# Kernel optimization log

Hardware: AMD Instinct MI355X
Metric: run time of the kernel (lower is better)

## Reference

```python
import jax, jax.numpy as jnp
import numpy as np

B, C, T, F = 64, 128, 2048, 5
ALPHA, BETA = 0.5, 0.5
N = C * F  # 640 nodes


def _spatial_adjacency():
    # |i-j| <= 3 neighbors within each frequency band block (block diagonal)
    idx = np.arange(C)
    d = np.abs(idx[:, None] - idx[None, :])
    blk = ((d <= 3) & (d > 0)).astype(np.float32)
    return jnp.asarray(np.kron(np.eye(F, dtype=np.float32), blk))


A_SPATIAL = _spatial_adjacency()  # (N, N)


def setup_inputs() -> dict:
    key = jax.random.key(0)
    ks = jax.random.split(key, 5)
    names = ['delta', 'theta', 'alpha', 'beta', 'gamma']
    return {n: jax.random.normal(k, (B, C, T), dtype=jnp.float32) for n, k in zip(names, ks)}


def _strg(delta, theta, alpha, beta, gamma):
    bands = jnp.stack([delta, theta, alpha, beta, gamma], axis=1)  # (B, F, C, T)
    Bn, Fn, Cn, Tn = bands.shape

    # bandpower = unbiased variance over time (torch.var default ddof=1)
    bp = jnp.var(bands, axis=3, ddof=1)  # (B, F, C)
    bandpowers = jnp.transpose(bp, (0, 2, 1))  # (B, C, F)
    # node ordering: node f*C + ch -> bandpowers[b, ch, f] == bp[b, f, ch]
    node_features = bp.reshape(Bn, Fn * Cn, 1)

    # Pearson-style functional connectivity per batch & band (vectorized)
    mean = jnp.mean(bands, axis=3, keepdims=True)
    std = jnp.std(bands, axis=3, ddof=1, keepdims=True)  # torch.std unbiased
    xn = (bands - mean) / (std + 1e-8)
    corr = jnp.einsum('bfct,bfdt->bfcd', xn, xn) / (Tn - 1)  # (B, F, C, C)
    corr = jnp.abs(corr)
    eye = jnp.eye(Cn, dtype=corr.dtype)
    corr = corr * (1.0 - eye) + eye  # zero diag, then set diag = 1
    corr = 0.5 * (corr + jnp.swapaxes(corr, 2, 3))

    # block-diagonal assembly into full functional adjacency
    A_func = jnp.zeros((Bn, N, N), dtype=corr.dtype)
    for f in range(Fn):
        s = f * Cn
        A_func = A_func.at[:, s:s + Cn, s:s + Cn].set(corr[:, f])

    A = ALPHA * A_SPATIAL[None] + BETA * A_func  # (B, N, N)

    # symmetric degree normalization D^-1/2 A D^-1/2
    D = jnp.sum(A, axis=2)
    d_inv_sqrt = (D + 1e-8) ** -0.5
    d_inv_sqrt = jnp.where(jnp.isinf(d_inv_sqrt), 0.0, d_inv_sqrt)
    A_norm = d_inv_sqrt[:, :, None] * A * d_inv_sqrt[:, None, :]

    return A_norm, node_features, bandpowers


def reference(delta, theta, alpha, beta, gamma):
    return _strg(delta, theta, alpha, beta, gamma)
```

## Files before the change

### kernel.cpp

```cpp
#include <hip/hip_runtime.h>
#include <hip/hip_bf16.h>

#define Bn 64
#define Cn 128
#define Tn 2048
#define Fn 5
#define Nn 640
#define TCHUNK 128
#define NCHUNK (Tn / TCHUNK)

typedef __attribute__((ext_vector_type(8))) short bf16x8;
typedef __attribute__((ext_vector_type(4))) float f32x4;

__device__ __forceinline__ short f2bf(float f) {
    union { float f; unsigned u; } v; v.f = f;
    unsigned r = (v.u + 0x7fffu + ((v.u >> 16) & 1u)) >> 16;
    return (short)r;
}

__device__ __forceinline__ int swz_off(int row, int bytecol) {
    return (row * 256 + bytecol) ^ ((row & 7) << 4);
}

__global__ __launch_bounds__(512)
void strg_kernel(const float* __restrict__ d0, const float* __restrict__ d1,
                 const float* __restrict__ d2, const float* __restrict__ d3,
                 const float* __restrict__ d4, float* __restrict__ out)
{
    __shared__ short  Xs[Cn * TCHUNK];
    __shared__ float  S_lds[Cn];
    __shared__ float  diag[Cn];
    __shared__ float  mrow[Cn];
    __shared__ float  ivrow[Cn];
    __shared__ float  D_lds[Cn];
    __shared__ float  dinv[Cn];

    const int tid = threadIdx.x;
    const int bfid = blockIdx.x;
    const int b = bfid / Fn;
    const int f = bfid - b * Fn;

    const float* src = (f == 0) ? d0 : (f == 1) ? d1 : (f == 2) ? d2 : (f == 3) ? d3 : d4;
    src += (size_t)b * Cn * Tn;

    if (tid < Cn) { S_lds[tid] = 0.0f; D_lds[tid] = 0.0f; }

    const int srow = tid >> 4;
    const int sseg = tid & 15;

    const int lane = tid & 63;
    const int w  = tid >> 6;
    const int wr = w >> 1;
    const int wc = w & 1;
    const int r0 = wr * 32;
    const int c0 = wc * 64;
    const int lg = lane >> 4;
    const int ll = lane & 15;

    f32x4 acc[2][4] = {};
    float psum[4] = {0.f, 0.f, 0.f, 0.f};

    for (int ch = 0; ch < NCHUNK; ++ch) {
        const float* cb = src + ch * TCHUNK;
        #pragma unroll
        for (int i = 0; i < 4; ++i) {
            const int row = i * 32 + srow;
            const float* rp = cb + (size_t)row * Tn + sseg * 8;
            float4 v0 = *(const float4*)rp;
            float4 v1 = *(const float4*)(rp + 4);
            psum[i] += v0.x + v0.y + v0.z + v0.w + v1.x + v1.y + v1.z + v1.w;
            bf16x8 h;
            h[0]=f2bf(v0.x); h[1]=f2bf(v0.y); h[2]=f2bf(v0.z); h[3]=f2bf(v0.w);
            h[4]=f2bf(v1.x); h[5]=f2bf(v1.y); h[6]=f2bf(v1.z); h[7]=f2bf(v1.w);
            *(bf16x8*)((char*)Xs + swz_off(row, sseg * 16)) = h;
        }
        __syncthreads();

        #pragma unroll
        for (int ks = 0; ks < 4; ++ks) {
            bf16x8 afr[2], bfr[4];
            #pragma unroll
            for (int m = 0; m < 2; ++m) {
                const int row = r0 + m * 16 + ll;
                afr[m] = *(const bf16x8*)((const char*)Xs + swz_off(row, ks * 64 + lg * 16));
            }
            #pragma unroll
            for (int n = 0; n < 4; ++n) {
                const int col = c0 + n * 16 + ll;
                bfr[n] = *(const bf16x8*)((const char*)Xs + swz_off(col, ks * 64 + lg * 16));
            }
            #pragma unroll
            for (int m = 0; m < 2; ++m)
                #pragma unroll
                for (int n = 0; n < 4; ++n)
                    acc[m][n] = __builtin_amdgcn_mfma_f32_16x16x32_bf16(afr[m], bfr[n], acc[m][n], 0, 0, 0);
        }
        __syncthreads();
    }

    #pragma unroll
    for (int i = 0; i < 4; ++i)
        atomicAdd(&S_lds[i * 32 + srow], psum[i]);

    #pragma unroll
    for (int m = 0; m < 2; ++m)
      #pragma unroll
      for (int n = 0; n < 4; ++n)
        #pragma unroll
        for (int e = 0; e < 4; ++e) {
            const int row = r0 + m * 16 + lg * 4 + e;
            const int col = c0 + n * 16 + ll;
            if (row == col) diag[row] = acc[m][n][e];
        }
    __syncthreads();

    if (tid < Cn) {
        const float S  = S_lds[tid];
        const float mu = S * (1.0f / Tn);
        float var = (diag[tid] - (float)Tn * mu * mu) * (1.0f / (Tn - 1));
        var = var < 0.f ? 0.f : var;
        const float sd = sqrtf(var);
        mrow[tid]  = mu;
        ivrow[tid] = 1.0f / (sd + 1e-8f);
        const size_t ofs = (size_t)Bn * Nn * Nn;
        out[ofs + (size_t)b * Nn + f * Cn + tid] = var;
        out[ofs + (size_t)Bn * Nn + ((size_t)b * Cn + tid) * Fn + f] = var;
    }
    __syncthreads();

    float mi[2][4], ii[2][4], mj[4], ij[4];
    #pragma unroll
    for (int m = 0; m < 2; ++m)
      #pragma unroll
      for (int e = 0; e < 4; ++e) {
          const int row = r0 + m * 16 + lg * 4 + e;
          mi[m][e] = mrow[row];
          ii[m][e] = ivrow[row];
      }
    #pragma unroll
    for (int n = 0; n < 4; ++n) {
        const int col = c0 + n * 16 + ll;
        mj[n] = mrow[col];
        ij[n] = ivrow[col];
    }

    auto ablk = [&](int m, int n, int e) -> float {
        const int row = r0 + m * 16 + lg * 4 + e;
        const int col = c0 + n * 16 + ll;
        float c = fabsf((acc[m][n][e] - (float)Tn * mi[m][e] * mj[n])
                        * ii[m][e] * ij[n] * (1.0f / (Tn - 1)));
        c = (row == col) ? 1.0f : c;
        const int d = row > col ? row - col : col - row;
        const float spa = (d >= 1 && d <= 3) ? 1.0f : 0.0f;
        return 0.5f * (spa + c);
    };

    #pragma unroll
    for (int m = 0; m < 2; ++m)
      #pragma unroll
      for (int e = 0; e < 4; ++e) {
          float s = 0.f;
          #pragma unroll
          for (int n = 0; n < 4; ++n) s += ablk(m, n, e);
          s += __shfl_xor(s, 1);
          s += __shfl_xor(s, 2);
          s += __shfl_xor(s, 4);
          s += __shfl_xor(s, 8);
          if (ll == 0) atomicAdd(&D_lds[r0 + m * 16 + lg * 4 + e], s);
      }
    __syncthreads();

    if (tid < Cn) dinv[tid] = rsqrtf(D_lds[tid] + 1e-8f);
    __syncthreads();

    float di[2][4], dj[4];
    #pragma unroll
    for (int m = 0; m < 2; ++m)
      #pragma unroll
      for (int e = 0; e < 4; ++e)
          di[m][e] = dinv[r0 + m * 16 + lg * 4 + e];
    #pragma unroll
    for (int n = 0; n < 4; ++n)
        dj[n] = dinv[c0 + n * 16 + ll];

    float* Ab = out + (size_t)b * Nn * Nn;
    const int fc = f * Cn;
    #pragma unroll
    for (int m = 0; m < 2; ++m)
      #pragma unroll
      for (int e = 0; e < 4; ++e) {
          const int row = r0 + m * 16 + lg * 4 + e;
          const size_t rowoff = (size_t)(fc + row) * Nn + fc;
          #pragma unroll
          for (int n = 0; n < 4; ++n) {
              const int col = c0 + n * 16 + ll;
              Ab[rowoff + col] = di[m][e] * ablk(m, n, e) * dj[n];
          }
      }
}

extern "C" void kernel_launch(void* const* d_in, const int* in_sizes, int n_in,
                              void* d_out, int out_size, void* d_ws, size_t ws_size,
                              hipStream_t stream) {
    const float* d0 = (const float*)d_in[0];
    const float* d1 = (const float*)d_in[1];
    const float* d2 = (const float*)d_in[2];
    const float* d3 = (const float*)d_in[3];
    const float* d4 = (const float*)d_in[4];
    float* out = (float*)d_out;

    hipMemsetAsync(d_out, 0, (size_t)out_size * sizeof(float), stream);

    strg_kernel<<<dim3(Bn * Fn), dim3(512), 0, stream>>>(d0, d1, d2, d3, d4, out);
}
```

Before: 113.5 us.

## Split Gram computation over time chunks and finalize in a separate kernel

```diff
diff --git a/kernel.cpp b/kernel.cpp
--- a/kernel.cpp
+++ b/kernel.cpp
@@ -7,7 +7,6 @@
 #define Fn 5
 #define Nn 640
 #define TCHUNK 128
-#define NCHUNK (Tn / TCHUNK)
 
 typedef __attribute__((ext_vector_type(8))) short bf16x8;
 typedef __attribute__((ext_vector_type(4))) float f32x4;
@@ -22,10 +21,213 @@
     return (row * 256 + bytecol) ^ ((row & 7) << 4);
 }
 
+__device__ __forceinline__ const float* pick_band(const float* d0, const float* d1,
+                                                  const float* d2, const float* d3,
+                                                  const float* d4, int f) {
+    return (f == 0) ? d0 : (f == 1) ? d1 : (f == 2) ? d2 : (f == 3) ? d3 : d4;
+}
+
+__global__ __launch_bounds__(512, 4)
+void gram_kernel(const float* __restrict__ d0, const float* __restrict__ d1,
+                 const float* __restrict__ d2, const float* __restrict__ d3,
+                 const float* __restrict__ d4,
+                 float* __restrict__ wsG, float* __restrict__ wsS, int Q)
+{
+    __shared__ short Xs[Cn * TCHUNK];
+    __shared__ float S_lds[Cn];
+
+    const int tid = threadIdx.x;
+    const int blk = blockIdx.x;
+    const int bf = blk / Q;
+    const int q  = blk - bf * Q;
+    const int b = bf / Fn;
+    const int f = bf - b * Fn;
+    const int NC = 16 / Q;
+
+    const float* src = pick_band(d0, d1, d2, d3, d4, f)
+                     + (size_t)b * Cn * Tn + (size_t)q * (Tn / Q);
+
+    if (tid < Cn) S_lds[tid] = 0.0f;
+
+    const int srow = tid >> 4;
+    const int sseg = tid & 15;
+
+    const int lane = tid & 63;
+    const int w  = tid >> 6;
+    const int wr = w >> 1;
+    const int wc = w & 1;
+    const int r0 = wr * 32;
+    const int c0 = wc * 64;
+    const int lg = lane >> 4;
+    const int ll = lane & 15;
+
+    f32x4 acc[2][4] = {};
+    float psum[4] = {0.f, 0.f, 0.f, 0.f};
+
+    float4 pf[8];
+    auto issue = [&](int ch) {
+        const float* cb = src + ch * TCHUNK;
+        #pragma unroll
+        for (int i = 0; i < 4; ++i) {
+            const float* rp = cb + (size_t)(i * 32 + srow) * Tn + sseg * 8;
+            pf[2 * i]     = *(const float4*)rp;
+            pf[2 * i + 1] = *(const float4*)(rp + 4);
+        }
+    };
+
+    issue(0);
+
+    for (int ch = 0; ch < NC; ++ch) {
+        #pragma unroll
+        for (int i = 0; i < 4; ++i) {
+            const int row = i * 32 + srow;
+            float4 v0 = pf[2 * i], v1 = pf[2 * i + 1];
+            psum[i] += v0.x + v0.y + v0.z + v0.w + v1.x + v1.y + v1.z + v1.w;
+            bf16x8 h;
+            h[0]=f2bf(v0.x); h[1]=f2bf(v0.y); h[2]=f2bf(v0.z); h[3]=f2bf(v0.w);
+            h[4]=f2bf(v1.x); h[5]=f2bf(v1.y); h[6]=f2bf(v1.z); h[7]=f2bf(v1.w);
+            *(bf16x8*)((char*)Xs + swz_off(row, sseg * 16)) = h;
+        }
+        if (ch + 1 < NC) issue(ch + 1);
+        __syncthreads();
+
+        #pragma unroll
+        for (int ks = 0; ks < 4; ++ks) {
+            bf16x8 afr[2], bfr[4];
+            #pragma unroll
+            for (int m = 0; m < 2; ++m) {
+                const int row = r0 + m * 16 + ll;
+                afr[m] = *(const bf16x8*)((const char*)Xs + swz_off(row, ks * 64 + lg * 16));
+            }
+            #pragma unroll
+            for (int n = 0; n < 4; ++n) {
+                const int col = c0 + n * 16 + ll;
+                bfr[n] = *(const bf16x8*)((const char*)Xs + swz_off(col, ks * 64 + lg * 16));
+            }
+            #pragma unroll
+            for (int m = 0; m < 2; ++m)
+                #pragma unroll
+                for (int n = 0; n < 4; ++n)
+                    acc[m][n] = __builtin_amdgcn_mfma_f32_16x16x32_bf16(afr[m], bfr[n], acc[m][n], 0, 0, 0);
+        }
+        __syncthreads();
+    }
+
+    #pragma unroll
+    for (int i = 0; i < 4; ++i)
+        atomicAdd(&S_lds[i * 32 + srow], psum[i]);
+    __syncthreads();
+    if (tid < Cn) wsS[(size_t)blk * Cn + tid] = S_lds[tid];
+
+    float* G = wsG + (size_t)blk * (Cn * Cn);
+    #pragma unroll
+    for (int m = 0; m < 2; ++m)
+      #pragma unroll
+      for (int e = 0; e < 4; ++e) {
+          const int row = r0 + m * 16 + lg * 4 + e;
+          #pragma unroll
+          for (int n = 0; n < 4; ++n) {
+              const int col = c0 + n * 16 + ll;
+              G[row * Cn + col] = acc[m][n][e];
+          }
+      }
+}
+
+__global__ __launch_bounds__(256)
+void finalize_kernel(const float* __restrict__ wsG, const float* __restrict__ wsS,
+                     float* __restrict__ out, int Q)
+{
+    __shared__ float G[Cn * Cn];
+    __shared__ float mrow[Cn], ivrow[Cn], dinv_s[Cn], Dsum[Cn];
+
+    const int tid = threadIdx.x;
+    const int bf = blockIdx.x;
+    const int b = bf / Fn;
+    const int f = bf - b * Fn;
+
+    const float* P0 = wsG + (size_t)bf * Q * (Cn * Cn);
+    for (int e = 0; e < 16; ++e) {
+        const int idx = e * 1024 + tid * 4;
+        float4 s = *(const float4*)(P0 + idx);
+        for (int qq = 1; qq < Q; ++qq) {
+            float4 t = *(const float4*)(P0 + (size_t)qq * (Cn * Cn) + idx);
+            s.x += t.x; s.y += t.y; s.z += t.z; s.w += t.w;
+        }
+        *(float4*)&G[idx] = s;
+    }
+
+    float S = 0.f;
+    if (tid < Cn) {
+        const float* Sp = wsS + (size_t)bf * Q * Cn;
+        for (int qq = 0; qq < Q; ++qq) S += Sp[qq * Cn + tid];
+        Dsum[tid] = 0.f;
+    }
+    __syncthreads();
+
+    if (tid < Cn) {
+        const float mu = S * (1.0f / Tn);
+        float var = (G[tid * (Cn + 1)] - (float)Tn * mu * mu) * (1.0f / (Tn - 1));
+        var = var < 0.f ? 0.f : var;
+        const float sd = sqrtf(var);
+        mrow[tid]  = mu;
+        ivrow[tid] = 1.0f / (sd + 1e-8f);
+        const size_t ofs = (size_t)Bn * Nn * Nn;
+        out[ofs + (size_t)b * Nn + f * Cn + tid] = var;
+        out[ofs + (size_t)Bn * Nn + ((size_t)b * Cn + tid) * Fn + f] = var;
+    }
+    __syncthreads();
+
+    const float inv = 1.0f / (Tn - 1);
+    for (int e = 0; e < 64; ++e) {
+        const int idx = e * 256 + tid;
+        const int row = idx >> 7;
+        const int col = idx & 127;
+        const float qv = G[idx];
+        float c = fabsf((qv - (float)Tn * mrow[row] * mrow[col]) * ivrow[row] * ivrow[col] * inv);
+        c = (row == col) ? 1.0f : c;
+        const int d = row > col ? row - col : col - row;
+        const float spa = (d >= 1 && d <= 3) ? 1.0f : 0.0f;
+        const float a = 0.5f * (spa + c);
+        G[idx] = a;
+        float s = a;
+        s += __shfl_xor(s, 1);
+        s += __shfl_xor(s, 2);
+        s += __shfl_xor(s, 4);
+        s += __shfl_xor(s, 8);
+        s += __shfl_xor(s, 16);
+        s += __shfl_xor(s, 32);
+        if ((tid & 63) == 0) atomicAdd(&Dsum[row], s);
+    }
+    __syncthreads();
+
+    if (tid < Cn) dinv_s[tid] = rsqrtf(Dsum[tid] + 1e-8f);
+    __syncthreads();
+
+    float* Ob = out + (size_t)b * Nn * Nn;
+    const int fc = f * Cn;
+    for (int e = 0; e < 80; ++e) {
+        const int idx4 = e * 1024 + tid * 4;
+        const int row = idx4 / Nn;
+        const int col = idx4 - row * Nn;
+        const int cl = col - fc;
+        float4 v;
+        if (cl >= 0 && cl < Cn) {
+            const float dr = dinv_s[row];
+            v.x = dr * G[row * Cn + cl]     * dinv_s[cl];
+            v.y = dr * G[row * Cn + cl + 1] * dinv_s[cl + 1];
+            v.z = dr * G[row * Cn + cl + 2] * dinv_s[cl + 2];
+            v.w = dr * G[row * Cn + cl + 3] * dinv_s[cl + 3];
+        } else {
+            v.x = 0.f; v.y = 0.f; v.z = 0.f; v.w = 0.f;
+        }
+        *(float4*)(Ob + (size_t)(fc + row) * Nn + col) = v;
+    }
+}
+
 __global__ __launch_bounds__(512)
-void strg_kernel(const float* __restrict__ d0, const float* __restrict__ d1,
-                 const float* __restrict__ d2, const float* __restrict__ d3,
-                 const float* __restrict__ d4, float* __restrict__ out)
+void strg_fallback(const float* __restrict__ d0, const float* __restrict__ d1,
+                   const float* __restrict__ d2, const float* __restrict__ d3,
+                   const float* __restrict__ d4, float* __restrict__ out)
 {
     __shared__ short  Xs[Cn * TCHUNK];
     __shared__ float  S_lds[Cn];
@@ -40,14 +242,12 @@
     const int b = bfid / Fn;
     const int f = bfid - b * Fn;
 
-    const float* src = (f == 0) ? d0 : (f == 1) ? d1 : (f == 2) ? d2 : (f == 3) ? d3 : d4;
-    src += (size_t)b * Cn * Tn;
+    const float* src = pick_band(d0, d1, d2, d3, d4, f) + (size_t)b * Cn * Tn;
 
     if (tid < Cn) { S_lds[tid] = 0.0f; D_lds[tid] = 0.0f; }
 
     const int srow = tid >> 4;
     const int sseg = tid & 15;
-
     const int lane = tid & 63;
     const int w  = tid >> 6;
     const int wr = w >> 1;
@@ -60,7 +260,7 @@
     f32x4 acc[2][4] = {};
     float psum[4] = {0.f, 0.f, 0.f, 0.f};
 
-    for (int ch = 0; ch < NCHUNK; ++ch) {
+    for (int ch = 0; ch < 16; ++ch) {
         const float* cb = src + ch * TCHUNK;
         #pragma unroll
         for (int i = 0; i < 4; ++i) {
@@ -75,20 +275,15 @@
             *(bf16x8*)((char*)Xs + swz_off(row, sseg * 16)) = h;
         }
         __syncthreads();
-
         #pragma unroll
         for (int ks = 0; ks < 4; ++ks) {
             bf16x8 afr[2], bfr[4];
             #pragma unroll
-            for (int m = 0; m < 2; ++m) {
-                const int row = r0 + m * 16 + ll;
-                afr[m] = *(const bf16x8*)((const char*)Xs + swz_off(row, ks * 64 + lg * 16));
-            }
-            #pragma unroll
-            for (int n = 0; n < 4; ++n) {
-                const int col = c0 + n * 16 + ll;
-                bfr[n] = *(const bf16x8*)((const char*)Xs + swz_off(col, ks * 64 + lg * 16));
-            }
+            for (int m = 0; m < 2; ++m)
+                afr[m] = *(const bf16x8*)((const char*)Xs + swz_off(r0 + m * 16 + ll, ks * 64 + lg * 16));
+            #pragma unroll
+            for (int n = 0; n < 4; ++n)
+                bfr[n] = *(const bf16x8*)((const char*)Xs + swz_off(c0 + n * 16 + ll, ks * 64 + lg * 16));
             #pragma unroll
             for (int m = 0; m < 2; ++m)
                 #pragma unroll
@@ -209,7 +404,19 @@
     const float* d4 = (const float*)d_in[4];
     float* out = (float*)d_out;
 
-    hipMemsetAsync(d_out, 0, (size_t)out_size * sizeof(float), stream);
-
-    strg_kernel<<<dim3(Bn * Fn), dim3(512), 0, stream>>>(d0, d1, d2, d3, d4, out);
-}
+    int Q = 0;
+    for (int cand = 4; cand >= 1; cand >>= 1) {
+        size_t need = (size_t)320 * cand * (Cn * Cn + Cn) * sizeof(float);
+        if (need <= ws_size) { Q = cand; break; }
+    }
+
+    if (Q > 0) {
+        float* wsG = (float*)d_ws;
+        float* wsS = wsG + (size_t)320 * Q * (Cn * Cn);
+        gram_kernel<<<dim3(320 * Q), dim3(512), 0, stream>>>(d0, d1, d2, d3, d4, wsG, wsS, Q);
+        finalize_kernel<<<dim3(320), dim3(256), 0, stream>>>(wsG, wsS, out, Q);
+    } else {
+        hipMemsetAsync(d_out, 0, (size_t)out_size * sizeof(float), stream);
+        strg_fallback<<<dim3(320), dim3(512), 0, stream>>>(d0, d1, d2, d3, d4, out);
+    }
+}
```

Result: slower. 170.8 us (+50.6%).

## Double-buffer input staging and fuse zero-fill into coalesced output writes

Applied to the files above, without the earlier changes.

```diff
diff --git a/kernel.cpp b/kernel.cpp
--- a/kernel.cpp
+++ b/kernel.cpp
@@ -7,7 +7,8 @@
 #define Fn 5
 #define Nn 640
 #define TCHUNK 128
-#define NCHUNK (Tn / TCHUNK)
+#define NCHUNK 16
+#define BUFBYTES (Cn * TCHUNK * 2)
 
 typedef __attribute__((ext_vector_type(8))) short bf16x8;
 typedef __attribute__((ext_vector_type(4))) float f32x4;
@@ -22,28 +23,27 @@
     return (row * 256 + bytecol) ^ ((row & 7) << 4);
 }
 
-__global__ __launch_bounds__(512)
-void strg_kernel(const float* __restrict__ d0, const float* __restrict__ d1,
-                 const float* __restrict__ d2, const float* __restrict__ d3,
-                 const float* __restrict__ d4, float* __restrict__ out)
+__device__ __forceinline__ const float* pick_band(const float* d0, const float* d1,
+                                                  const float* d2, const float* d3,
+                                                  const float* d4, int f) {
+    return (f == 0) ? d0 : (f == 1) ? d1 : (f == 2) ? d2 : (f == 3) ? d3 : d4;
+}
+
+__global__ __launch_bounds__(512, 4)
+void strg_mono(const float* __restrict__ d0, const float* __restrict__ d1,
+               const float* __restrict__ d2, const float* __restrict__ d3,
+               const float* __restrict__ d4, float* __restrict__ out)
 {
-    __shared__ short  Xs[Cn * TCHUNK];
-    __shared__ float  S_lds[Cn];
-    __shared__ float  diag[Cn];
-    __shared__ float  mrow[Cn];
-    __shared__ float  ivrow[Cn];
-    __shared__ float  D_lds[Cn];
-    __shared__ float  dinv[Cn];
+    __shared__ __align__(16) char smem[2 * BUFBYTES];
+    __shared__ float S_lds[Cn], diag[Cn], mrow[Cn], ivrow[Cn], Dsum[Cn], dinv_s[Cn];
 
     const int tid = threadIdx.x;
     const int bfid = blockIdx.x;
     const int b = bfid / Fn;
     const int f = bfid - b * Fn;
-
-    const float* src = (f == 0) ? d0 : (f == 1) ? d1 : (f == 2) ? d2 : (f == 3) ? d3 : d4;
-    src += (size_t)b * Cn * Tn;
-
-    if (tid < Cn) { S_lds[tid] = 0.0f; D_lds[tid] = 0.0f; }
+    const float* src = pick_band(d0, d1, d2, d3, d4, f) + (size_t)b * Cn * Tn;
+
+    if (tid < Cn) { S_lds[tid] = 0.0f; Dsum[tid] = 0.0f; }
 
     const int srow = tid >> 4;
     const int sseg = tid & 15;
@@ -59,43 +59,68 @@
 
     f32x4 acc[2][4] = {};
     float psum[4] = {0.f, 0.f, 0.f, 0.f};
-
-    for (int ch = 0; ch < NCHUNK; ++ch) {
-        const float* cb = src + ch * TCHUNK;
+    float4 pf[8];
+
+    const float* tb0 = src + (size_t)srow * Tn + sseg * 8;
+
+    auto issue = [&](int ch) {
+        const float* cb = tb0 + ch * TCHUNK;
+        #pragma unroll
+        for (int i = 0; i < 4; ++i) {
+            const float* rp = cb + (size_t)(i * 32) * Tn;
+            pf[2 * i]     = *(const float4*)rp;
+            pf[2 * i + 1] = *(const float4*)(rp + 4);
+        }
+    };
+    auto convert_write = [&](int buf) {
+        char* base = smem + buf * BUFBYTES;
         #pragma unroll
         for (int i = 0; i < 4; ++i) {
             const int row = i * 32 + srow;
-            const float* rp = cb + (size_t)row * Tn + sseg * 8;
-            float4 v0 = *(const float4*)rp;
-            float4 v1 = *(const float4*)(rp + 4);
+            float4 v0 = pf[2 * i], v1 = pf[2 * i + 1];
             psum[i] += v0.x + v0.y + v0.z + v0.w + v1.x + v1.y + v1.z + v1.w;
             bf16x8 h;
             h[0]=f2bf(v0.x); h[1]=f2bf(v0.y); h[2]=f2bf(v0.z); h[3]=f2bf(v0.w);
             h[4]=f2bf(v1.x); h[5]=f2bf(v1.y); h[6]=f2bf(v1.z); h[7]=f2bf(v1.w);
-            *(bf16x8*)((char*)Xs + swz_off(row, sseg * 16)) = h;
-        }
-        __syncthreads();
-
+            *(bf16x8*)(base + swz_off(row, sseg * 16)) = h;
+        }
+    };
+    auto mfma_phase = [&](int buf) {
+        const char* base = smem + buf * BUFBYTES;
         #pragma unroll
         for (int ks = 0; ks < 4; ++ks) {
             bf16x8 afr[2], bfr[4];
             #pragma unroll
-            for (int m = 0; m < 2; ++m) {
-                const int row = r0 + m * 16 + ll;
-                afr[m] = *(const bf16x8*)((const char*)Xs + swz_off(row, ks * 64 + lg * 16));
-            }
+            for (int m = 0; m < 2; ++m)
+                afr[m] = *(const bf16x8*)(base + swz_off(r0 + m * 16 + ll, ks * 64 + lg * 16));
             #pragma unroll
-            for (int n = 0; n < 4; ++n) {
-                const int col = c0 + n * 16 + ll;
-                bfr[n] = *(const bf16x8*)((const char*)Xs + swz_off(col, ks * 64 + lg * 16));
-            }
+            for (int n = 0; n < 4; ++n)
+                bfr[n] = *(const bf16x8*)(base + swz_off(c0 + n * 16 + ll, ks * 64 + lg * 16));
             #pragma unroll
             for (int m = 0; m < 2; ++m)
                 #pragma unroll
                 for (int n = 0; n < 4; ++n)
                     acc[m][n] = __builtin_amdgcn_mfma_f32_16x16x32_bf16(afr[m], bfr[n], acc[m][n], 0, 0, 0);
         }
-        __syncthreads();
+    };
+
+    issue(0);
+    convert_write(0);
+    issue(1);
+    asm volatile("s_waitcnt lgkmcnt(0)" ::: "memory");
+    __builtin_amdgcn_s_barrier();
+    __builtin_amdgcn_sched_barrier(0);
+
+    for (int ch = 0; ch < NCHUNK; ++ch) {
+        const int cur = ch & 1;
+        mfma_phase(cur);
+        if (ch + 1 < NCHUNK) {
+            convert_write(cur ^ 1);
+            if (ch + 2 < NCHUNK) issue(ch + 2);
+        }
+        asm volatile("s_waitcnt lgkmcnt(0)" ::: "memory");
+        __builtin_amdgcn_s_barrier();
+        __builtin_amdgcn_sched_barrier(0);
     }
 
     #pragma unroll
@@ -128,75 +153,71 @@
     }
     __syncthreads();
 
-    float mi[2][4], ii[2][4], mj[4], ij[4];
-    #pragma unroll
-    for (int m = 0; m < 2; ++m)
-      #pragma unroll
-      for (int e = 0; e < 4; ++e) {
-          const int row = r0 + m * 16 + lg * 4 + e;
-          mi[m][e] = mrow[row];
-          ii[m][e] = ivrow[row];
-      }
-    #pragma unroll
-    for (int n = 0; n < 4; ++n) {
-        const int col = c0 + n * 16 + ll;
-        mj[n] = mrow[col];
-        ij[n] = ivrow[col];
-    }
-
-    auto ablk = [&](int m, int n, int e) -> float {
-        const int row = r0 + m * 16 + lg * 4 + e;
-        const int col = c0 + n * 16 + ll;
-        float c = fabsf((acc[m][n][e] - (float)Tn * mi[m][e] * mj[n])
-                        * ii[m][e] * ij[n] * (1.0f / (Tn - 1)));
-        c = (row == col) ? 1.0f : c;
-        const int d = row > col ? row - col : col - row;
-        const float spa = (d >= 1 && d <= 3) ? 1.0f : 0.0f;
-        return 0.5f * (spa + c);
-    };
-
-    #pragma unroll
-    for (int m = 0; m < 2; ++m)
-      #pragma unroll
-      for (int e = 0; e < 4; ++e) {
-          float s = 0.f;
+    float* At = (float*)smem;
+    {
+        float mi[2][4], ii[2][4], mj[4], ij[4];
+        #pragma unroll
+        for (int m = 0; m < 2; ++m)
           #pragma unroll
-          for (int n = 0; n < 4; ++n) s += ablk(m, n, e);
-          s += __shfl_xor(s, 1);
-          s += __shfl_xor(s, 2);
-          s += __shfl_xor(s, 4);
-          s += __shfl_xor(s, 8);
-          if (ll == 0) atomicAdd(&D_lds[r0 + m * 16 + lg * 4 + e], s);
-      }
-    __syncthreads();
-
-    if (tid < Cn) dinv[tid] = rsqrtf(D_lds[tid] + 1e-8f);
-    __syncthreads();
-
-    float di[2][4], dj[4];
-    #pragma unroll
-    for (int m = 0; m < 2; ++m)
-      #pragma unroll
-      for (int e = 0; e < 4; ++e)
-          di[m][e] = dinv[r0 + m * 16 + lg * 4 + e];
-    #pragma unroll
-    for (int n = 0; n < 4; ++n)
-        dj[n] = dinv[c0 + n * 16 + ll];
-
-    float* Ab = out + (size_t)b * Nn * Nn;
+          for (int e = 0; e < 4; ++e) {
+              const int row = r0 + m * 16 + lg * 4 + e;
+              mi[m][e] = mrow[row];
+              ii[m][e] = ivrow[row];
+          }
+        #pragma unroll
+        for (int n = 0; n < 4; ++n) {
+            const int col = c0 + n * 16 + ll;
+            mj[n] = mrow[col];
+            ij[n] = ivrow[col];
+        }
+        const float inv = 1.0f / (Tn - 1);
+        #pragma unroll
+        for (int m = 0; m < 2; ++m)
+          #pragma unroll
+          for (int e = 0; e < 4; ++e) {
+              const int row = r0 + m * 16 + lg * 4 + e;
+              float s = 0.f;
+              #pragma unroll
+              for (int n = 0; n < 4; ++n) {
+                  const int col = c0 + n * 16 + ll;
+                  float c = fabsf((acc[m][n][e] - (float)Tn * mi[m][e] * mj[n])
+                                  * ii[m][e] * ij[n] * inv);
+                  c = (row == col) ? 1.0f : c;
+                  const int d = row > col ? row - col : col - row;
+                  const float spa = (d >= 1 && d <= 3) ? 1.0f : 0.0f;
+                  const float a = 0.5f * (spa + c);
+                  At[row * Cn + col] = a;
+                  s += a;
+              }
+              s += __shfl_xor(s, 1);
+              s += __shfl_xor(s, 2);
+              s += __shfl_xor(s, 4);
+              s += __shfl_xor(s, 8);
+              if (ll == 0) atomicAdd(&Dsum[row], s);
+          }
+    }
+    __syncthreads();
+
+    if (tid < Cn) dinv_s[tid] = rsqrtf(Dsum[tid] + 1e-8f);
+    __syncthreads();
+
+    float* Ob = out + (size_t)b * Nn * Nn;
     const int fc = f * Cn;
-    #pragma unroll
-    for (int m = 0; m < 2; ++m)
-      #pragma unroll
-      for (int e = 0; e < 4; ++e) {
-          const int row = r0 + m * 16 + lg * 4 + e;
-          const size_t rowoff = (size_t)(fc + row) * Nn + fc;
-          #pragma unroll
-          for (int n = 0; n < 4; ++n) {
-              const int col = c0 + n * 16 + ll;
-              Ab[rowoff + col] = di[m][e] * ablk(m, n, e) * dj[n];
-          }
-      }
+    for (int e = 0; e < 40; ++e) {
+        const int idx4 = e * 2048 + tid * 4;
+        const int row = idx4 / Nn;
+        const int col = idx4 - row * Nn;
+        const int cl = col - fc;
+        float4 v = {0.f, 0.f, 0.f, 0.f};
+        if (cl >= 0 && cl < Cn) {
+            const float dr = dinv_s[row];
+            v.x = dr * At[row * Cn + cl]     * dinv_s[cl];
+            v.y = dr * At[row * Cn + cl + 1] * dinv_s[cl + 1];
+            v.z = dr * At[row * Cn + cl + 2] * dinv_s[cl + 2];
+            v.w = dr * At[row * Cn + cl + 3] * dinv_s[cl + 3];
+        }
+        *(float4*)(Ob + (size_t)(fc + row) * Nn + col) = v;
+    }
 }
 
 extern "C" void kernel_launch(void* const* d_in, const int* in_sizes, int n_in,
@@ -209,7 +230,5 @@
     const float* d4 = (const float*)d_in[4];
     float* out = (float*)d_out;
 
-    hipMemsetAsync(d_out, 0, (size_t)out_size * sizeof(float), stream);
-
-    strg_kernel<<<dim3(Bn * Fn), dim3(512), 0, stream>>>(d0, d1, d2, d3, d4, out);
-}
+    strg_mono<<<dim3(Bn * Fn), dim3(512), 0, stream>>>(d0, d1, d2, d3, d4, out);
+}
```

Result: no change. 115.1 us (+1.5%).
